# Optimization experiments

Measured on AMD Instinct MI355X. Metric: run time of the kernel, lower is better.

Reference implementation:

```python
import jax, jax.numpy as jnp
import numpy as np

N_HEAD = 8


def setup_inputs() -> dict:
    key = jax.random.key(0)
    ks = jax.random.split(key, 4)
    B, L, C = 4, 1024, 512
    x = jax.random.normal(ks[0], (B, L, C), dtype=jnp.float32)
    adj = jax.random.uniform(ks[1], (B, L, L), dtype=jnp.float32)
    W_qkv = jax.random.normal(ks[2], (3 * C, C), dtype=jnp.float32) * 0.02
    W_proj = jax.random.normal(ks[3], (C, C), dtype=jnp.float32) * 0.02
    bias_scale = jnp.array([3.0, 3.0], dtype=jnp.float32)
    beta = jnp.ones((3,), dtype=jnp.float32) / 3.0
    return {"x": x, "adj": adj, "W_qkv": W_qkv, "W_proj": W_proj,
            "bias_scale": bias_scale, "beta": beta}


def _branch_attn(Q, K, V, scale, bias=None):
    # Q,K,V: [B,H,L,D]
    S = jnp.einsum('bhqd,bhkd->bhqk', Q, K) / scale
    if bias is not None:
        S = S + bias
    attn = jax.nn.softmax(S, axis=-1)
    return jnp.einsum('bhqk,bhkd->bhqd', attn, V)


def reference(x, adj, W_qkv, W_proj, bias_scale, beta):
    B, L, C = x.shape
    H = N_HEAD
    D = C // H
    scale = jnp.sqrt(jnp.float32(D))

    qkv = x @ W_qkv.T  # [B,L,3C]
    Q, K, V = jnp.split(qkv, 3, axis=-1)
    Q = Q.reshape(B, L, H, D).transpose(0, 2, 1, 3)  # [B,H,L,D]
    K = K.reshape(B, L, H, D).transpose(0, 2, 1, 3)
    V = V.reshape(B, L, H, D).transpose(0, 2, 1, 3)

    # has_cls: zero out CLS row/col in adjacency
    adj_local = adj.at[:, 0, :].set(0.0).at[:, :, 0].set(0.0)
    B_fwd = adj_local[:, None, :, :]              # [B,1,L,L]
    B_bwd = jnp.swapaxes(adj_local, -1, -2)[:, None, :, :]

    h0 = _branch_attn(Q, K, V, scale)
    h1 = _branch_attn(Q, K, V, scale, bias_scale[0] * B_fwd)
    h2 = _branch_attn(Q, K, V, scale, bias_scale[1] * B_bwd)

    b = jax.nn.softmax(beta, axis=0)
    out = b[0] * h0 + b[1] * h1 + b[2] * h2      # [B,H,L,D]
    out = out.transpose(0, 2, 1, 3).reshape(B, L, C)
    return out @ W_proj.T
```

## Files before the change

kernel.cpp:

```cpp
#include <hip/hip_runtime.h>
#include <hip/hip_bf16.h>
#include <stdint.h>

#define B_  4
#define L_  1024
#define C_  512
#define D_  64
#define BH_ 32
#define M_  4096

typedef short  bf16x8 __attribute__((ext_vector_type(8)));
typedef float  f32x4  __attribute__((ext_vector_type(4)));
typedef unsigned short u16x8 __attribute__((ext_vector_type(8)));
typedef unsigned int   u32x2 __attribute__((ext_vector_type(2)));

__device__ __forceinline__ unsigned short f2bf(float f) {
    union { float f; uint32_t u; } v; v.f = f;
    uint32_t u = v.u;
    return (unsigned short)((u + 0x7fffu + ((u >> 16) & 1u)) >> 16);
}
__device__ __forceinline__ float bf2f(unsigned short s) {
    union { uint32_t u; float f; } v; v.u = ((uint32_t)s) << 16;
    return v.f;
}

__device__ __forceinline__ void gload16(const void* g, void* s) {
    __builtin_amdgcn_global_load_lds((const __attribute__((address_space(1))) void*)g,
                                     (__attribute__((address_space(3))) void*)s, 16, 0, 0);
}

#define NX4   (M_ * C_ / 4)
#define NWQ4  (3 * C_ * C_ / 4)
#define NWP4  (C_ * C_ / 4)
__global__ void cvt_all(const float* __restrict__ x, const float* __restrict__ wq,
                        const float* __restrict__ wp,
                        unsigned short* __restrict__ xb, unsigned short* __restrict__ wqb,
                        unsigned short* __restrict__ wpb) {
    int i = blockIdx.x * 256 + threadIdx.x;
    const float* src; unsigned short* dst; int o;
    if (i < NX4) { src = x; dst = xb; o = i; }
    else if (i < NX4 + NWQ4) { src = wq; dst = wqb; o = i - NX4; }
    else if (i < NX4 + NWQ4 + NWP4) { src = wp; dst = wpb; o = i - NX4 - NWQ4; }
    else return;
    float4 v = ((const float4*)src)[o];
    ushort4 r;
    r.x = f2bf(v.x); r.y = f2bf(v.y); r.z = f2bf(v.z); r.w = f2bf(v.w);
    ((ushort4*)dst)[o] = r;
}

__global__ __launch_bounds__(256) void prep_e(const float* __restrict__ adj,
                                              const float* __restrict__ bias_scale,
                                              unsigned short* __restrict__ EI) {
    __shared__ float Tr[64][65];
    const int b = blockIdx.z, q0 = blockIdx.y * 64, k0 = blockIdx.x * 64;
    const float* adjb = adj + (size_t)b * L_ * L_;
    const int tid = threadIdx.x;
#pragma unroll
    for (int i = 0; i < 4; ++i) {
        int idx = i * 256 + tid;
        int rk = idx >> 4, c4 = (idx & 15) * 4;
        float4 v = *(const float4*)(adjb + (size_t)(k0 + rk) * L_ + q0 + c4);
        Tr[rk][c4 + 0] = v.x; Tr[rk][c4 + 1] = v.y; Tr[rk][c4 + 2] = v.z; Tr[rk][c4 + 3] = v.w;
    }
    __syncthreads();
    const float bs0 = bias_scale[0], bs1 = bias_scale[1];
    const int w = tid >> 6, l = tid & 63, g = l >> 4, c = l & 15;
#pragma unroll
    for (int qs = 0; qs < 4; ++qs) {
        int ql = qs * 16 + c, qg = q0 + ql;
        int klb = w * 16 + g * 4;
        float4 af4 = *(const float4*)(adjb + (size_t)qg * L_ + k0 + klb);
        unsigned short ef[4], eb[4];
        const float afv[4] = {af4.x, af4.y, af4.z, af4.w};
#pragma unroll
        for (int e = 0; e < 4; ++e) {
            int kg = k0 + klb + e;
            bool z = (qg == 0) || (kg == 0);
            ef[e] = f2bf(z ? 1.0f : __expf(bs0 * afv[e]));
            eb[e] = f2bf(z ? 1.0f : __expf(bs1 * Tr[klb + e][ql]));
        }
        size_t o = (((size_t)b * 64 + (blockIdx.y * 4 + qs)) * 64 + (blockIdx.x * 4 + w)) * 512 + (size_t)l * 8;
        *(u16x8*)(EI + o) = (u16x8){ef[0], ef[1], ef[2], ef[3], eb[0], eb[1], eb[2], eb[3]};
    }
}

template <int BM, int BN, int KDIM, int EPI, int NDIM>
__global__ __launch_bounds__(256, 4) void gemm_bf16(const unsigned short* __restrict__ Amat,
                                                    const unsigned short* __restrict__ Bmat,
                                                    float* __restrict__ outp,
                                                    unsigned short* __restrict__ q_out,
                                                    unsigned short* __restrict__ k_out,
                                                    unsigned short* __restrict__ v_out) {
    constexpr int NA = BM / 32, NB = BN / 32;
    constexpr int MI = BM / 32, NI = BN / 32;
    __shared__ __align__(16) unsigned short As[BM * 64];
    __shared__ __align__(16) unsigned short Bs[BN * 64];
    const int tid = threadIdx.x;
    const int l = tid & 63, wid = tid >> 6;
    const int g = l >> 4, c = l & 15;
    const int wr = wid >> 1, wc = wid & 1;
    const int row0 = blockIdx.y * BM, col0 = blockIdx.x * BN;

    f32x4 acc[MI][NI];
#pragma unroll
    for (int mi = 0; mi < MI; ++mi)
#pragma unroll
        for (int ni = 0; ni < NI; ++ni) acc[mi][ni] = (f32x4){0.f, 0.f, 0.f, 0.f};

    for (int k0 = 0; k0 < KDIM; k0 += 64) {
        bf16x8 ra[NA], rb[NB];
#pragma unroll
        for (int i = 0; i < NA; ++i) {
            int q = i * 256 + tid;
            int r = q >> 3, cb = (q & 7) * 16;
            ra[i] = *(const bf16x8*)((const char*)Amat + (size_t)(row0 + r) * (KDIM * 2) + k0 * 2 + cb);
        }
#pragma unroll
        for (int i = 0; i < NB; ++i) {
            int q = i * 256 + tid;
            int r = q >> 3, cb = (q & 7) * 16;
            rb[i] = *(const bf16x8*)((const char*)Bmat + (size_t)(col0 + r) * (KDIM * 2) + k0 * 2 + cb);
        }
        __syncthreads();
#pragma unroll
        for (int i = 0; i < NA; ++i) {
            int q = i * 256 + tid;
            int r = q >> 3, cb = (q & 7) * 16;
            *(bf16x8*)((char*)As + r * 128 + (cb ^ ((r & 7) << 4))) = ra[i];
        }
#pragma unroll
        for (int i = 0; i < NB; ++i) {
            int q = i * 256 + tid;
            int r = q >> 3, cb = (q & 7) * 16;
            *(bf16x8*)((char*)Bs + r * 128 + (cb ^ ((r & 7) << 4))) = rb[i];
        }
        __syncthreads();
#pragma unroll
        for (int kk = 0; kk < 2; ++kk) {
            bf16x8 afr[MI], bfr[NI];
#pragma unroll
            for (int mi = 0; mi < MI; ++mi) {
                int r = wr * (BM / 2) + mi * 16 + c;
                afr[mi] = *(const bf16x8*)((const char*)As + r * 128 + ((kk * 64 + g * 16) ^ ((r & 7) << 4)));
            }
#pragma unroll
            for (int ni = 0; ni < NI; ++ni) {
                int r = wc * (BN / 2) + ni * 16 + c;
                bfr[ni] = *(const bf16x8*)((const char*)Bs + r * 128 + ((kk * 64 + g * 16) ^ ((r & 7) << 4)));
            }
#pragma unroll
            for (int mi = 0; mi < MI; ++mi)
#pragma unroll
                for (int ni = 0; ni < NI; ++ni)
                    acc[mi][ni] = __builtin_amdgcn_mfma_f32_16x16x32_bf16(afr[mi], bfr[ni], acc[mi][ni], 0, 0, 0);
        }
    }
#pragma unroll
    for (int mi = 0; mi < MI; ++mi) {
#pragma unroll
        for (int ni = 0; ni < NI; ++ni) {
#pragma unroll
            for (int ii = 0; ii < 4; ++ii) {
                int m = row0 + wr * (BM / 2) + mi * 16 + g * 4 + ii;
                int n = col0 + wc * (BN / 2) + ni * 16 + c;
                float val = acc[mi][ni][ii];
                if (EPI == 0) {
                    unsigned short v = f2bf(val);
                    int b = m >> 10, ll = m & 1023;
                    int which = n >> 9, cc = n & 511;
                    int hh = cc >> 6, d = cc & 63;
                    int bh = b * 8 + hh;
                    if (which == 0)      q_out[((size_t)bh * L_ + ll) * D_ + d] = v;
                    else if (which == 1) k_out[((size_t)bh * L_ + ll) * D_ + d] = v;
                    else                 v_out[((size_t)bh * D_ + d) * L_ + ll] = v;
                } else {
                    outp[(size_t)m * NDIM + n] = val;
                }
            }
        }
    }
}

struct EReg { bf16x8 e[8]; };

__global__ __launch_bounds__(256, 2) void attn_kernel(const unsigned short* __restrict__ Qb,
                                                      const unsigned short* __restrict__ Kb,
                                                      const unsigned short* __restrict__ Vtb,
                                                      const unsigned short* __restrict__ EI,
                                                      const float* __restrict__ beta,
                                                      unsigned short* __restrict__ hb) {
    __shared__ __align__(16) char smem[2][32768];
    const int tid = threadIdx.x;
    const int w = tid >> 6, l = tid & 63;
    const int g = l >> 4, c = l & 15;

    const int p = blockIdx.x;
    const int s = (p & 7) + 8 * (p >> 6);
    const int h = (p >> 3) & 7;
    const int b = s >> 4, qb = s & 15;
    const int bh = b * 8 + h;
    const int q0 = qb * 64 + w * 16;
    const int qt = qb * 4 + w;

    const unsigned short* Qrow = Qb + ((size_t)bh * L_ + q0 + c) * D_;
    const bf16x8 qf0 = *(const bf16x8*)(Qrow + g * 8);
    const bf16x8 qf1 = *(const bf16x8*)(Qrow + 32 + g * 8);

    const unsigned short* Kbase = Kb + (size_t)bh * L_ * D_;
    const unsigned short* Vbase = Vtb + (size_t)bh * D_ * L_;
    const unsigned short* Ebase = EI + ((size_t)(b * 64 + qt) * 64) * 512;

    f32x4 O[3][4];
#pragma unroll
    for (int j = 0; j < 3; ++j)
#pragma unroll
        for (int dc = 0; dc < 4; ++dc) O[j][dc] = (f32x4){0.f, 0.f, 0.f, 0.f};
    float lsum0 = 0.f, lsum1 = 0.f, lsum2 = 0.f;

    const int srow = l >> 3, sm = l & 7;
    const int key = (c & 7) << 4;

    auto stage = [&](int t, char* base) {
#pragma unroll
        for (int n = 0; n < 2; ++n) {
            int i = 2 * w + n;
            int row = i * 8 + srow;
            int sw = (sm ^ (row & 7)) * 8;
            gload16(Kbase + (size_t)(t * 128 + row) * D_ + sw,      base +         i * 1024);
            gload16(Kbase + (size_t)(t * 128 + 64 + row) * D_ + sw, base +  8192 + i * 1024);
            gload16(Vbase + (size_t)row * L_ + t * 128 + sw,        base + 16384 + i * 1024);
            gload16(Vbase + (size_t)row * L_ + t * 128 + 64 + sw,   base + 24576 + i * 1024);
        }
    };
    auto eload = [&](EReg& X, int t) {
#pragma unroll
        for (int ks = 0; ks < 8; ++ks)
            X.e[ks] = *(const bf16x8*)(Ebase + (size_t)(t * 8 + ks) * 512 + l * 8);
    };

    auto compute64 = [&](const char* Kl, const char* Vl,
                         bf16x8 ee0, bf16x8 ee1, bf16x8 ee2, bf16x8 ee3) {
        bf16x8 earr[4] = {ee0, ee1, ee2, ee3};
        unsigned rr[4][3][2];
#pragma unroll
        for (int st = 0; st < 4; ++st) {
            const char* kr = Kl + (st * 16 + c) * 128;
            bf16x8 ka = *(const bf16x8*)(kr + ((g * 16) ^ key));
            bf16x8 kb = *(const bf16x8*)(kr + ((64 + g * 16) ^ key));
            f32x4 sacc = (f32x4){0.f, 0.f, 0.f, 0.f};
            sacc = __builtin_amdgcn_mfma_f32_16x16x32_bf16(ka, qf0, sacc, 0, 0, 0);
            sacc = __builtin_amdgcn_mfma_f32_16x16x32_bf16(kb, qf1, sacc, 0, 0, 0);
            float pv[3][4];
#pragma unroll
            for (int i = 0; i < 4; ++i) {
                float p0 = __expf(sacc[i] * 0.125f);
                float p1 = p0 * bf2f((unsigned short)earr[st][i]);
                float p2 = p0 * bf2f((unsigned short)earr[st][4 + i]);
                lsum0 += p0; lsum1 += p1; lsum2 += p2;
                pv[0][i] = p0; pv[1][i] = p1; pv[2][i] = p2;
            }
#pragma unroll
            for (int j = 0; j < 3; ++j) {
                rr[st][j][0] = __builtin_amdgcn_perm(__float_as_uint(pv[j][1]), __float_as_uint(pv[j][0]), 0x07060302u);
                rr[st][j][1] = __builtin_amdgcn_perm(__float_as_uint(pv[j][3]), __float_as_uint(pv[j][2]), 0x07060302u);
            }
        }
#pragma unroll
        for (int kk = 0; kk < 2; ++kk) {
            bf16x8 af[3];
#pragma unroll
            for (int j = 0; j < 3; ++j) {
                union { unsigned u[4]; bf16x8 v; } t_;
                t_.u[0] = rr[2 * kk][j][0];     t_.u[1] = rr[2 * kk][j][1];
                t_.u[2] = rr[2 * kk + 1][j][0]; t_.u[3] = rr[2 * kk + 1][j][1];
                af[j] = t_.v;
            }
#pragma unroll
            for (int dc = 0; dc < 4; ++dc) {
                const char* vr = Vl + (dc * 16 + c) * 128;
                u32x2 vlo = *(const u32x2*)(vr + ((kk * 64 + g * 8) ^ key));
                u32x2 vhi = *(const u32x2*)(vr + ((kk * 64 + 32 + g * 8) ^ key));
                union { unsigned u[4]; bf16x8 v; } bv;
                bv.u[0] = vlo[0]; bv.u[1] = vlo[1]; bv.u[2] = vhi[0]; bv.u[3] = vhi[1];
#pragma unroll
                for (int j = 0; j < 3; ++j)
                    O[j][dc] = __builtin_amdgcn_mfma_f32_16x16x32_bf16(af[j], bv.v, O[j][dc], 0, 0, 0);
            }
        }
    };

    auto compute = [&](char* base, const EReg& E) {
        compute64(base,        base + 16384, E.e[0], E.e[1], E.e[2], E.e[3]);
        compute64(base + 8192, base + 24576, E.e[4], E.e[5], E.e[6], E.e[7]);
    };

    EReg E0, E1;
    stage(0, smem[0]);
    eload(E0, 0);
    __syncthreads();
#pragma unroll 1
    for (int t = 0; t < 8; t += 2) {
        stage(t + 1, smem[1]);
        eload(E1, t + 1);
        compute(smem[0], E0);
        __syncthreads();
        if (t + 2 < 8) { stage(t + 2, smem[0]); eload(E0, t + 2); }
        compute(smem[1], E1);
        __syncthreads();
    }

    lsum0 += __shfl_xor(lsum0, 16); lsum0 += __shfl_xor(lsum0, 32);
    lsum1 += __shfl_xor(lsum1, 16); lsum1 += __shfl_xor(lsum1, 32);
    lsum2 += __shfl_xor(lsum2, 16); lsum2 += __shfl_xor(lsum2, 32);

    float b0 = beta[0], b1 = beta[1], b2 = beta[2];
    float bm = fmaxf(b0, fmaxf(b1, b2));
    float e0 = __expf(b0 - bm), e1 = __expf(b1 - bm), e2 = __expf(b2 - bm);
    float inv = 1.0f / (e0 + e1 + e2);
    float i0 = e0 * inv / lsum0, i1 = e1 * inv / lsum1, i2 = e2 * inv / lsum2;

    float iq0[4], iq1[4], iq2[4];
#pragma unroll
    for (int ii = 0; ii < 4; ++ii) {
        iq0[ii] = __shfl(i0, g * 4 + ii);
        iq1[ii] = __shfl(i1, g * 4 + ii);
        iq2[ii] = __shfl(i2, g * 4 + ii);
    }
    const int hcol = (bh & 7) * 64;
#pragma unroll
    for (int dc = 0; dc < 4; ++dc) {
#pragma unroll
        for (int ii = 0; ii < 4; ++ii) {
            float hv = iq0[ii] * O[0][dc][ii] + iq1[ii] * O[1][dc][ii] + iq2[ii] * O[2][dc][ii];
            int qrow = q0 + g * 4 + ii;
            hb[((size_t)(b << 10) + qrow) * C_ + hcol + dc * 16 + c] = f2bf(hv);
        }
    }
}

extern "C" void kernel_launch(void* const* d_in, const int* in_sizes, int n_in,
                              void* d_out, int out_size, void* d_ws, size_t ws_size,
                              hipStream_t stream) {
    const float* x          = (const float*)d_in[0];
    const float* adj        = (const float*)d_in[1];
    const float* wqkv       = (const float*)d_in[2];
    const float* wproj      = (const float*)d_in[3];
    const float* bias_scale = (const float*)d_in[4];
    const float* beta       = (const float*)d_in[5];
    float* out = (float*)d_out;

    char* ws = (char*)d_ws;
    size_t off = 0;
    auto alloc = [&](size_t bytes) {
        void* p = ws + off;
        off += (bytes + 255) & ~(size_t)255;
        return p;
    };
    unsigned short* xb     = (unsigned short*)alloc((size_t)M_ * C_ * 2);
    unsigned short* wqkvb  = (unsigned short*)alloc((size_t)3 * C_ * C_ * 2);
    unsigned short* wprojb = (unsigned short*)alloc((size_t)C_ * C_ * 2);
    unsigned short* Qb     = (unsigned short*)alloc((size_t)BH_ * L_ * D_ * 2);
    unsigned short* Kb     = (unsigned short*)alloc((size_t)BH_ * L_ * D_ * 2);
    unsigned short* Vtb    = (unsigned short*)alloc((size_t)BH_ * D_ * L_ * 2);
    unsigned short* EI     = (unsigned short*)alloc((size_t)B_ * L_ * L_ * 4);
    unsigned short* hb     = (unsigned short*)alloc((size_t)M_ * C_ * 2);

    cvt_all<<<(NX4 + NWQ4 + NWP4 + 255) / 256, 256, 0, stream>>>(x, wqkv, wproj, xb, wqkvb, wprojb);
    prep_e<<<dim3(L_ / 64, L_ / 64, B_), 256, 0, stream>>>(adj, bias_scale, EI);
    gemm_bf16<64, 128, 512, 0, 0><<<dim3(1536 / 128, M_ / 64), 256, 0, stream>>>(xb, wqkvb, nullptr, Qb, Kb, Vtb);
    attn_kernel<<<dim3(512), 256, 0, stream>>>(Qb, Kb, Vtb, EI, beta, hb);
    gemm_bf16<64, 64, 512, 1, 512><<<dim3(512 / 64, M_ / 64), 256, 0, stream>>>(hb, wprojb, out, nullptr, nullptr, nullptr);
}
```

Measured before the change: 77.21 us.

## Split attention key range across two wave groups with LDS reduction

Attention blocks grow to 512 threads, and two groups of four waves each process half of the key sequence for the same 64 queries. Each group uses its own half-size shared-memory staging buffers. Afterward the second group writes its partial outputs and row sums to LDS, and the first group adds them in before normalization. This doubles the waves per block to raise latency hiding and occupancy with only 512 blocks, at the cost of an extra LDS reduction and sync.

```diff
diff --git a/kernel.cpp b/kernel.cpp
--- a/kernel.cpp
+++ b/kernel.cpp
@@ -181,17 +181,18 @@
     }
 }
 
-struct EReg { bf16x8 e[8]; };
-
-__global__ __launch_bounds__(256, 2) void attn_kernel(const unsigned short* __restrict__ Qb,
+struct EReg { bf16x8 e[4]; };
+
+__global__ __launch_bounds__(512, 4) void attn_kernel(const unsigned short* __restrict__ Qb,
                                                       const unsigned short* __restrict__ Kb,
                                                       const unsigned short* __restrict__ Vtb,
                                                       const unsigned short* __restrict__ EI,
                                                       const float* __restrict__ beta,
                                                       unsigned short* __restrict__ hb) {
-    __shared__ __align__(16) char smem[2][32768];
+    __shared__ __align__(16) char smem[2][2][16384];
     const int tid = threadIdx.x;
     const int w = tid >> 6, l = tid & 63;
+    const int half = w >> 2, wq = w & 3;
     const int g = l >> 4, c = l & 15;
 
     const int p = blockIdx.x;
@@ -199,8 +200,10 @@
     const int h = (p >> 3) & 7;
     const int b = s >> 4, qb = s & 15;
     const int bh = b * 8 + h;
-    const int q0 = qb * 64 + w * 16;
-    const int qt = qb * 4 + w;
+    const int q0 = qb * 64 + wq * 16;
+    const int qt = qb * 4 + wq;
+    const int kofs = half * 512;
+    const int e16 = half * 32;
 
     const unsigned short* Qrow = Qb + ((size_t)bh * L_ + q0 + c) * D_;
     const bf16x8 qf0 = *(const bf16x8*)(Qrow + g * 8);
@@ -223,24 +226,22 @@
     auto stage = [&](int t, char* base) {
 #pragma unroll
         for (int n = 0; n < 2; ++n) {
-            int i = 2 * w + n;
+            int i = 2 * wq + n;
             int row = i * 8 + srow;
             int sw = (sm ^ (row & 7)) * 8;
-            gload16(Kbase + (size_t)(t * 128 + row) * D_ + sw,      base +         i * 1024);
-            gload16(Kbase + (size_t)(t * 128 + 64 + row) * D_ + sw, base +  8192 + i * 1024);
-            gload16(Vbase + (size_t)row * L_ + t * 128 + sw,        base + 16384 + i * 1024);
-            gload16(Vbase + (size_t)row * L_ + t * 128 + 64 + sw,   base + 24576 + i * 1024);
+            gload16(Kbase + (size_t)(kofs + t * 64 + row) * D_ + sw, base + i * 1024);
+            gload16(Vbase + (size_t)row * L_ + kofs + t * 64 + sw, base + 8192 + i * 1024);
         }
     };
     auto eload = [&](EReg& X, int t) {
 #pragma unroll
-        for (int ks = 0; ks < 8; ++ks)
-            X.e[ks] = *(const bf16x8*)(Ebase + (size_t)(t * 8 + ks) * 512 + l * 8);
+        for (int ks = 0; ks < 4; ++ks)
+            X.e[ks] = *(const bf16x8*)(Ebase + (size_t)(e16 + t * 4 + ks) * 512 + l * 8);
     };
 
-    auto compute64 = [&](const char* Kl, const char* Vl,
-                         bf16x8 ee0, bf16x8 ee1, bf16x8 ee2, bf16x8 ee3) {
-        bf16x8 earr[4] = {ee0, ee1, ee2, ee3};
+    auto compute = [&](const char* base, const EReg& E) {
+        const char* Kl = base;
+        const char* Vl = base + 8192;
         unsigned rr[4][3][2];
 #pragma unroll
         for (int st = 0; st < 4; ++st) {
@@ -254,8 +255,8 @@
 #pragma unroll
             for (int i = 0; i < 4; ++i) {
                 float p0 = __expf(sacc[i] * 0.125f);
-                float p1 = p0 * bf2f((unsigned short)earr[st][i]);
-                float p2 = p0 * bf2f((unsigned short)earr[st][4 + i]);
+                float p1 = p0 * bf2f((unsigned short)E.e[st][i]);
+                float p2 = p0 * bf2f((unsigned short)E.e[st][4 + i]);
                 lsum0 += p0; lsum1 += p1; lsum2 += p2;
                 pv[0][i] = p0; pv[1][i] = p1; pv[2][i] = p2;
             }
@@ -289,25 +290,47 @@
         }
     };
 
-    auto compute = [&](char* base, const EReg& E) {
-        compute64(base,        base + 16384, E.e[0], E.e[1], E.e[2], E.e[3]);
-        compute64(base + 8192, base + 24576, E.e[4], E.e[5], E.e[6], E.e[7]);
-    };
-
     EReg E0, E1;
-    stage(0, smem[0]);
+    stage(0, smem[0][half]);
     eload(E0, 0);
     __syncthreads();
 #pragma unroll 1
     for (int t = 0; t < 8; t += 2) {
-        stage(t + 1, smem[1]);
+        stage(t + 1, smem[1][half]);
         eload(E1, t + 1);
-        compute(smem[0], E0);
+        compute(smem[0][half], E0);
         __syncthreads();
-        if (t + 2 < 8) { stage(t + 2, smem[0]); eload(E0, t + 2); }
-        compute(smem[1], E1);
+        if (t + 2 < 8) { stage(t + 2, smem[0][half]); eload(E0, t + 2); }
+        compute(smem[1][half], E1);
         __syncthreads();
     }
+
+    float* cb = (float*)&smem[0][0][0];
+    float* lb = cb + 4 * 48 * 64;
+    if (half == 1) {
+#pragma unroll
+        for (int j = 0; j < 3; ++j)
+#pragma unroll
+            for (int dc = 0; dc < 4; ++dc)
+#pragma unroll
+                for (int ii = 0; ii < 4; ++ii)
+                    cb[(wq * 48 + j * 16 + dc * 4 + ii) * 64 + l] = O[j][dc][ii];
+        lb[(wq * 3 + 0) * 64 + l] = lsum0;
+        lb[(wq * 3 + 1) * 64 + l] = lsum1;
+        lb[(wq * 3 + 2) * 64 + l] = lsum2;
+    }
+    __syncthreads();
+    if (half == 1) return;
+#pragma unroll
+    for (int j = 0; j < 3; ++j)
+#pragma unroll
+        for (int dc = 0; dc < 4; ++dc)
+#pragma unroll
+            for (int ii = 0; ii < 4; ++ii)
+                O[j][dc][ii] += cb[(wq * 48 + j * 16 + dc * 4 + ii) * 64 + l];
+    lsum0 += lb[(wq * 3 + 0) * 64 + l];
+    lsum1 += lb[(wq * 3 + 1) * 64 + l];
+    lsum2 += lb[(wq * 3 + 2) * 64 + l];
 
     lsum0 += __shfl_xor(lsum0, 16); lsum0 += __shfl_xor(lsum0, 32);
     lsum1 += __shfl_xor(lsum1, 16); lsum1 += __shfl_xor(lsum1, 32);
@@ -368,6 +391,6 @@
     cvt_all<<<(NX4 + NWQ4 + NWP4 + 255) / 256, 256, 0, stream>>>(x, wqkv, wproj, xb, wqkvb, wprojb);
     prep_e<<<dim3(L_ / 64, L_ / 64, B_), 256, 0, stream>>>(adj, bias_scale, EI);
     gemm_bf16<64, 128, 512, 0, 0><<<dim3(1536 / 128, M_ / 64), 256, 0, stream>>>(xb, wqkvb, nullptr, Qb, Kb, Vtb);
-    attn_kernel<<<dim3(512), 256, 0, stream>>>(Qb, Kb, Vtb, EI, beta, hb);
+    attn_kernel<<<dim3(512), 512, 0, stream>>>(Qb, Kb, Vtb, EI, beta, hb);
     gemm_bf16<64, 64, 512, 1, 512><<<dim3(512 / 64, M_ / 64), 256, 0, stream>>>(hb, wprojb, out, nullptr, nullptr, nullptr);
 }
```

After: 153.1 us. +98.3%, slower.
